# Kernel optimization log

Hardware: AMD Instinct MI355X
Metric: run time of the kernel (lower is better)

## Reference

```python
import jax, jax.numpy as jnp
import numpy as np

V = 1000      # output_dim (vocab)
H = 512       # hidden_dim
D = 512       # input_dim == d_model of MHA
HEADS = 8
DK = D // HEADS
MEM = 512     # memory_len
BS = 128      # batch
TMAX = 160    # max decode steps (== max(output_lens))


def setup_inputs() -> dict:
    key = jax.random.key(0)
    ks = jax.random.split(key, 16)
    s = 0.05
    f = lambda k, shape: jax.random.normal(k, shape, jnp.float32) * s
    memory = jax.random.normal(ks[0], (MEM, BS, D), jnp.float32)
    lens = jnp.sort(jax.random.randint(ks[1], (BS,), 1, TMAX + 1))[::-1]
    lens = lens.at[0].set(TMAX)  # torch runs max(output_lens) steps; pin to TMAX
    return dict(
        memory=memory,
        emb=f(ks[2], (V, H)),
        Wq=f(ks[3], (D, 2 * H)), bq=f(ks[4], (D,)),
        Wk=f(ks[5], (D, D)), bk=f(ks[6], (D,)),
        Wv=f(ks[7], (D, D)), bv=f(ks[8], (D,)),
        W_ih=f(ks[9], (3 * H, D)), W_hh=f(ks[10], (3 * H, H)),
        b_ih=f(ks[11], (3 * H,)), b_hh=f(ks[12], (3 * H,)),
        Wfc=f(ks[13], (V, H)), bfc=f(ks[14], (V,)),
        output_lens=lens,
    )


def _forward(memory, emb, Wq, bq, Wk, bk, Wv, bv, W_ih, W_hh, b_ih, b_hh, Wfc, bfc, output_lens):
    mem_len, bs, _ = memory.shape
    scale = 1.0 / np.sqrt(DK)
    # Precompute key/value projections once (memory is constant over decode steps).
    # (mem_len, bs, D) -> (bs, heads, mem_len, dk)
    kp = (memory @ Wk.T + bk).reshape(mem_len, bs, HEADS, DK).transpose(1, 2, 0, 3)
    vp = (memory @ Wv.T + bv).reshape(mem_len, bs, HEADS, DK).transpose(1, 2, 0, 3)

    def step(carry, i):
        out, hid = carry  # (bs, V), (bs, H)
        tok = jnp.argmax(out, axis=-1)                 # greedy feedback (annotations=None)
        q = jnp.concatenate([emb[tok], hid], axis=-1) @ Wq.T + bq  # (bs, D)
        qh = q.reshape(bs, HEADS, DK)
        att = jax.nn.softmax(jnp.einsum('bhd,bhmd->bhm', qh, kp) * scale, axis=-1)
        ctx = jnp.einsum('bhm,bhmd->bhd', att, vp).reshape(bs, D)
        # GRU cell (PyTorch gate order: r, z, n)
        gi = ctx @ W_ih.T + b_ih
        gh = hid @ W_hh.T + b_hh
        ir, iz, inn = jnp.split(gi, 3, axis=-1)
        hr, hz, hn = jnp.split(gh, 3, axis=-1)
        r = jax.nn.sigmoid(ir + hr)
        z = jax.nn.sigmoid(iz + hz)
        n = jnp.tanh(inn + r * hn)
        h_new = (1.0 - z) * n + z * hid
        o_new = h_new @ Wfc.T + bfc
        # Ragged masking: torch truncates finished batch items; each item is
        # independent, so masking the recorded outputs is equivalent.
        run = (i < output_lens)[:, None]
        ys = (jnp.where(run, o_new, 0.0),
              jnp.where(run, h_new, 0.0),
              jnp.where(run, att.mean(axis=1), 0.0))
        return (o_new, h_new), ys

    init = (jnp.zeros((bs, V), jnp.float32), jnp.zeros((bs, H), jnp.float32))
    _, (outputs, hiddens, scores) = jax.lax.scan(step, init, jnp.arange(TMAX))
    return outputs, hiddens, scores  # (T,bs,V), (T,bs,H), (T,bs,mem_len)


def reference(memory, emb, Wq, bq, Wk, bk, Wv, bv, W_ih, W_hh, b_ih, b_hh, Wfc, bfc, output_lens):
    return _forward(memory, emb, Wq, bq, Wk, bk, Wv, bv, W_ih, W_hh, b_ih, b_hh, Wfc, bfc, output_lens)
```

## Files before the change

### kernel.cpp

```cpp
#include <hip/hip_runtime.h>
#include <math.h>

__global__ __launch_bounds__(256) void kv_proj(
    const float* __restrict__ mem, const float* __restrict__ W,
    const float* __restrict__ bias, float* __restrict__ outp) {
  __shared__ float As[32][68];
  __shared__ float Bs[32][68];
  int gid = blockIdx.x;
  int jt = gid & 7, mt = (gid >> 3) & 7, b = gid >> 6;
  int t = threadIdx.x;
  int lm = t >> 2;
  int kq = (t & 3) * 8;
  int tx = t & 15, ty = t >> 4;
  float acc[4][4];
  #pragma unroll
  for (int r = 0; r < 4; ++r)
    #pragma unroll
    for (int c = 0; c < 4; ++c) acc[r][c] = 0.f;
  const float* Arow = mem + (size_t)(mt * 64 + lm) * 65536 + (size_t)b * 512 + kq;
  const float* Brow = W + (size_t)(jt * 64 + lm) * 512 + kq;
  for (int k0 = 0; k0 < 512; k0 += 32) {
    float4 a0 = *(const float4*)(Arow + k0);
    float4 a1 = *(const float4*)(Arow + k0 + 4);
    float4 b0 = *(const float4*)(Brow + k0);
    float4 b1 = *(const float4*)(Brow + k0 + 4);
    As[kq + 0][lm] = a0.x; As[kq + 1][lm] = a0.y; As[kq + 2][lm] = a0.z; As[kq + 3][lm] = a0.w;
    As[kq + 4][lm] = a1.x; As[kq + 5][lm] = a1.y; As[kq + 6][lm] = a1.z; As[kq + 7][lm] = a1.w;
    Bs[kq + 0][lm] = b0.x; Bs[kq + 1][lm] = b0.y; Bs[kq + 2][lm] = b0.z; Bs[kq + 3][lm] = b0.w;
    Bs[kq + 4][lm] = b1.x; Bs[kq + 5][lm] = b1.y; Bs[kq + 6][lm] = b1.z; Bs[kq + 7][lm] = b1.w;
    __syncthreads();
    #pragma unroll
    for (int k = 0; k < 32; ++k) {
      float4 av = *(const float4*)&As[k][ty * 4];
      float4 bv = *(const float4*)&Bs[k][tx * 4];
      float ar[4] = {av.x, av.y, av.z, av.w};
      float br[4] = {bv.x, bv.y, bv.z, bv.w};
      #pragma unroll
      for (int r = 0; r < 4; ++r)
        #pragma unroll
        for (int c = 0; c < 4; ++c) acc[r][c] = fmaf(ar[r], br[c], acc[r][c]);
    }
    __syncthreads();
  }
  float4 bb = *(const float4*)(bias + jt * 64 + tx * 4);
  #pragma unroll
  for (int r = 0; r < 4; ++r) {
    int m = mt * 64 + ty * 4 + r;
    float4 o;
    o.x = acc[r][0] + bb.x; o.y = acc[r][1] + bb.y;
    o.z = acc[r][2] + bb.z; o.w = acc[r][3] + bb.w;
    *(float4*)(outp + (((size_t)b * 8 + jt) * 512 + m) * 64 + tx * 4) = o;
  }
}

__global__ __launch_bounds__(256) void kv_projT(
    const float* __restrict__ mem, const float* __restrict__ W,
    const float* __restrict__ bias, float* __restrict__ outp) {
  __shared__ float As[32][68];
  __shared__ float Bs[32][68];
  int gid = blockIdx.x;
  int jt = gid & 7, mt = (gid >> 3) & 7, b = gid >> 6;
  int t = threadIdx.x;
  int lm = t >> 2;
  int kq = (t & 3) * 8;
  int tx = t & 15, ty = t >> 4;
  float acc[4][4];
  #pragma unroll
  for (int r = 0; r < 4; ++r)
    #pragma unroll
    for (int c = 0; c < 4; ++c) acc[r][c] = 0.f;
  const float* Arow = mem + (size_t)(mt * 64 + lm) * 65536 + (size_t)b * 512 + kq;
  const float* Brow = W + (size_t)(jt * 64 + lm) * 512 + kq;
  for (int k0 = 0; k0 < 512; k0 += 32) {
    float4 a0 = *(const float4*)(Arow + k0);
    float4 a1 = *(const float4*)(Arow + k0 + 4);
    float4 b0 = *(const float4*)(Brow + k0);
    float4 b1 = *(const float4*)(Brow + k0 + 4);
    As[kq + 0][lm] = a0.x; As[kq + 1][lm] = a0.y; As[kq + 2][lm] = a0.z; As[kq + 3][lm] = a0.w;
    As[kq + 4][lm] = a1.x; As[kq + 5][lm] = a1.y; As[kq + 6][lm] = a1.z; As[kq + 7][lm] = a1.w;
    Bs[kq + 0][lm] = b0.x; Bs[kq + 1][lm] = b0.y; Bs[kq + 2][lm] = b0.z; Bs[kq + 3][lm] = b0.w;
    Bs[kq + 4][lm] = b1.x; Bs[kq + 5][lm] = b1.y; Bs[kq + 6][lm] = b1.z; Bs[kq + 7][lm] = b1.w;
    __syncthreads();
    #pragma unroll
    for (int k = 0; k < 32; ++k) {
      float4 av = *(const float4*)&As[k][ty * 4];
      float4 bv = *(const float4*)&Bs[k][tx * 4];
      float ar[4] = {av.x, av.y, av.z, av.w};
      float br[4] = {bv.x, bv.y, bv.z, bv.w};
      #pragma unroll
      for (int r = 0; r < 4; ++r)
        #pragma unroll
        for (int c = 0; c < 4; ++c) acc[r][c] = fmaf(ar[r], br[c], acc[r][c]);
    }
    __syncthreads();
  }
  float4 bb = *(const float4*)(bias + jt * 64 + tx * 4);
  float bc[4] = {bb.x, bb.y, bb.z, bb.w};
  #pragma unroll
  for (int r = 0; r < 4; ++r) {
    int m = mt * 64 + ty * 4 + r;
    #pragma unroll
    for (int c = 0; c < 4; ++c) {
      int d = tx * 4 + c;
      outp[((size_t)(b * 8 + jt) * 64 + d) * 512 + m] = acc[r][c] + bc[c];
    }
  }
}

__global__ __launch_bounds__(256) void init_kernel(float* __restrict__ h0,
                                                   unsigned long long* __restrict__ packed) {
  int t = threadIdx.x + blockIdx.x * blockDim.x;
  for (int i = t; i < 128 * 512; i += blockDim.x * gridDim.x) h0[i] = 0.f;
  if (t < 128) packed[t] = (0x80000000ull << 32) | 0xFFFFFFFFull;
}

__global__ __launch_bounds__(256) void attn_fused(
    const float* __restrict__ kpT, const float* __restrict__ vp,
    const float* __restrict__ emb, const float* __restrict__ Wq,
    const float* __restrict__ bq, const unsigned long long* __restrict__ packed,
    const float* __restrict__ h_prev, float* __restrict__ ctx,
    float* __restrict__ att_buf) {
  int b = blockIdx.x >> 3, hd = blockIdx.x & 7;
  __shared__ float act[1024];
  __shared__ float qs[64];
  __shared__ float att[512];
  __shared__ __align__(16) float red[16][68];
  __shared__ float rmax[4], rsum[4];
  __shared__ int tok_s;
  int t = threadIdx.x;
  if (t == 0) tok_s = (int)(0xFFFFFFFFu - (unsigned int)(packed[b] & 0xFFFFFFFFull));
  __syncthreads();
  int tok = tok_s;
  act[t]       = emb[(size_t)tok * 512 + t];
  act[256 + t] = emb[(size_t)tok * 512 + 256 + t];
  act[512 + t] = h_prev[(size_t)b * 512 + t];
  act[768 + t] = h_prev[(size_t)b * 512 + 256 + t];
  __syncthreads();

  {
    int jl = t >> 2, kc = t & 3;
    const float* wrow = Wq + (size_t)(hd * 64 + jl) * 1024 + kc * 256;
    const float* a = act + kc * 256;
    float p = 0.f;
    #pragma unroll 8
    for (int i = 0; i < 256; i += 4) {
      float4 w = *(const float4*)(wrow + i);
      p = fmaf(a[i + 0], w.x, p);
      p = fmaf(a[i + 1], w.y, p);
      p = fmaf(a[i + 2], w.z, p);
      p = fmaf(a[i + 3], w.w, p);
    }
    p += __shfl_xor(p, 1);
    p += __shfl_xor(p, 2);
    if (kc == 0) qs[jl] = p + bq[hd * 64 + jl];
  }
  __syncthreads();

  const float* Kb = kpT + (size_t)(b * 8 + hd) * 32768;
  float s0 = 0.f, s1 = 0.f;
  {
    int m2 = 2 * t;
    #pragma unroll 8
    for (int d = 0; d < 64; ++d) {
      float2 kk = *(const float2*)(Kb + (size_t)d * 512 + m2);
      float qd = qs[d];
      s0 = fmaf(qd, kk.x, s0);
      s1 = fmaf(qd, kk.y, s1);
    }
    s0 *= 0.125f;
    s1 *= 0.125f;
  }
  float mx = fmaxf(s0, s1);
  #pragma unroll
  for (int o = 32; o > 0; o >>= 1) mx = fmaxf(mx, __shfl_xor(mx, o));
  if ((t & 63) == 0) rmax[t >> 6] = mx;
  __syncthreads();
  mx = fmaxf(fmaxf(rmax[0], rmax[1]), fmaxf(rmax[2], rmax[3]));
  float e0 = expf(s0 - mx), e1 = expf(s1 - mx);
  float sm = e0 + e1;
  #pragma unroll
  for (int o = 32; o > 0; o >>= 1) sm += __shfl_xor(sm, o);
  if ((t & 63) == 0) rsum[t >> 6] = sm;
  __syncthreads();
  sm = rsum[0] + rsum[1] + rsum[2] + rsum[3];
  float inv = 1.f / sm;
  float a0 = e0 * inv, a1 = e1 * inv;
  att[2 * t] = a0;
  att[2 * t + 1] = a1;
  *(float2*)(att_buf + (size_t)(b * 8 + hd) * 512 + 2 * t) = make_float2(a0, a1);
  __syncthreads();

  const float* Vb = vp + (size_t)(b * 8 + hd) * 32768;
  {
    int dsl = (t & 15) * 4, g = t >> 4;
    float c0 = 0.f, c1 = 0.f, c2 = 0.f, c3 = 0.f;
    #pragma unroll 4
    for (int m = g; m < 512; m += 16) {
      float4 vv = *(const float4*)(Vb + (size_t)m * 64 + dsl);
      float am = att[m];
      c0 = fmaf(am, vv.x, c0);
      c1 = fmaf(am, vv.y, c1);
      c2 = fmaf(am, vv.z, c2);
      c3 = fmaf(am, vv.w, c3);
    }
    red[g][dsl + 0] = c0;
    red[g][dsl + 1] = c1;
    red[g][dsl + 2] = c2;
    red[g][dsl + 3] = c3;
  }
  __syncthreads();
  if (t < 64) {
    float cc = 0.f;
    #pragma unroll
    for (int g2 = 0; g2 < 16; ++g2) cc += red[g2][t];
    ctx[(size_t)b * 512 + hd * 64 + t] = cc;
  }
}

__global__ __launch_bounds__(256) void gru_kernel(
    const float* __restrict__ W_ih, const float* __restrict__ W_hh,
    const float* __restrict__ b_ih, const float* __restrict__ b_hh,
    const float* __restrict__ ctx, const float* __restrict__ h_prev,
    float* __restrict__ h_new, const float* __restrict__ att_buf,
    const int* __restrict__ lens, float* __restrict__ out_hid,
    float* __restrict__ out_sc, unsigned long long* __restrict__ packed,
    int step) {
  __shared__ float cs[8][512];
  __shared__ float hs[8][512];
  int bi = blockIdx.x;
  int t = threadIdx.x;
  if (bi >= 256) {
    int sb = bi - 256;
    if (sb == 0 && t < 128) packed[t] = 0ull;
    #pragma unroll
    for (int i = 0; i < 4; ++i) {
      int flat = sb * 1024 + i * 256 + t;
      int bb = flat >> 9, m = flat & 511;
      float sum = 0.f;
      #pragma unroll
      for (int h = 0; h < 8; ++h) sum += att_buf[(size_t)(bb * 8 + h) * 512 + m];
      float val = sum * 0.125f;
      out_sc[(size_t)step * 65536 + flat] = (step < lens[bb]) ? val : 0.f;
    }
    return;
  }
  int bt = bi >> 4, jt = bi & 15;
  #pragma unroll
  for (int i = 0; i < 16; ++i) {
    int flat = i * 256 + t;
    int lb = flat >> 9, k = flat & 511;
    cs[lb][k] = ctx[(size_t)(bt * 8 + lb) * 512 + k];
    hs[lb][k] = h_prev[(size_t)(bt * 8 + lb) * 512 + k];
  }
  __syncthreads();
  int lb = t >> 5, j = (jt << 5) + (t & 31);
  int b = bt * 8 + lb;
  float air = b_ih[j], aiz = b_ih[512 + j], ain = b_ih[1024 + j];
  float ahr = b_hh[j], ahz = b_hh[512 + j], ahn = b_hh[1024 + j];
  const float* c = cs[lb];
  const float* hh = hs[lb];
  const float* wi0 = W_ih + (size_t)j * 512;
  const float* wi1 = W_ih + (size_t)(512 + j) * 512;
  const float* wi2 = W_ih + (size_t)(1024 + j) * 512;
  const float* wh0 = W_hh + (size_t)j * 512;
  const float* wh1 = W_hh + (size_t)(512 + j) * 512;
  const float* wh2 = W_hh + (size_t)(1024 + j) * 512;
  #pragma unroll 2
  for (int k = 0; k < 512; k += 4) {
    float4 wa = *(const float4*)(wi0 + k);
    float4 wb = *(const float4*)(wi1 + k);
    float4 wc = *(const float4*)(wi2 + k);
    float4 wd = *(const float4*)(wh0 + k);
    float4 we = *(const float4*)(wh1 + k);
    float4 wf = *(const float4*)(wh2 + k);
    float c0 = c[k], c1 = c[k + 1], c2 = c[k + 2], c3 = c[k + 3];
    float h0 = hh[k], h1 = hh[k + 1], h2 = hh[k + 2], h3 = hh[k + 3];
    air = fmaf(c0, wa.x, air); air = fmaf(c1, wa.y, air); air = fmaf(c2, wa.z, air); air = fmaf(c3, wa.w, air);
    aiz = fmaf(c0, wb.x, aiz); aiz = fmaf(c1, wb.y, aiz); aiz = fmaf(c2, wb.z, aiz); aiz = fmaf(c3, wb.w, aiz);
    ain = fmaf(c0, wc.x, ain); ain = fmaf(c1, wc.y, ain); ain = fmaf(c2, wc.z, ain); ain = fmaf(c3, wc.w, ain);
    ahr = fmaf(h0, wd.x, ahr); ahr = fmaf(h1, wd.y, ahr); ahr = fmaf(h2, wd.z, ahr); ahr = fmaf(h3, wd.w, ahr);
    ahz = fmaf(h0, we.x, ahz); ahz = fmaf(h1, we.y, ahz); ahz = fmaf(h2, we.z, ahz); ahz = fmaf(h3, we.w, ahz);
    ahn = fmaf(h0, wf.x, ahn); ahn = fmaf(h1, wf.y, ahn); ahn = fmaf(h2, wf.z, ahn); ahn = fmaf(h3, wf.w, ahn);
  }
  float r = 1.f / (1.f + expf(-(air + ahr)));
  float z = 1.f / (1.f + expf(-(aiz + ahz)));
  float n = tanhf(fmaf(r, ahn, ain));
  float hp = hh[j];
  float hv = (1.f - z) * n + z * hp;
  h_new[(size_t)b * 512 + j] = hv;
  out_hid[(size_t)step * 65536 + (size_t)b * 512 + j] = (step < lens[b]) ? hv : 0.f;
}

__global__ __launch_bounds__(256) void logits_kernel(
    const float* __restrict__ Wfc, const float* __restrict__ bfc,
    const float* __restrict__ h_new, const int* __restrict__ lens,
    float* __restrict__ out_o, unsigned long long* __restrict__ packed,
    int step) {
  __shared__ float hs[8][512];
  int bi = blockIdx.x;
  int t = threadIdx.x;
  int bt = bi >> 4, vt = bi & 15;
  #pragma unroll
  for (int i = 0; i < 16; ++i) {
    int flat = i * 256 + t;
    int lb = flat >> 9, k = flat & 511;
    hs[lb][k] = h_new[(size_t)(bt * 8 + lb) * 512 + k];
  }
  __syncthreads();
  int lb = t >> 5, vv = t & 31;
  int b = bt * 8 + lb;
  const float* a = hs[lb];
  int run = step < lens[b];
  float bestv = -1e30f;
  int besti = 0;
  #pragma unroll
  for (int r = 0; r < 2; ++r) {
    int v = vt * 64 + r * 32 + vv;
    if (v < 1000) {
      float acc = bfc[v];
      const float* wrow = Wfc + (size_t)v * 512;
      #pragma unroll 4
      for (int k = 0; k < 512; k += 4) {
        float4 w = *(const float4*)(wrow + k);
        acc = fmaf(a[k + 0], w.x, acc);
        acc = fmaf(a[k + 1], w.y, acc);
        acc = fmaf(a[k + 2], w.z, acc);
        acc = fmaf(a[k + 3], w.w, acc);
      }
      out_o[(size_t)step * 128000 + (size_t)b * 1000 + v] = run ? acc : 0.f;
      if (acc > bestv) { bestv = acc; besti = v; }
    }
  }
  #pragma unroll
  for (int o = 16; o > 0; o >>= 1) {
    float ov = __shfl_xor(bestv, o);
    int oi = __shfl_xor(besti, o);
    if (ov > bestv || (ov == bestv && oi < besti)) { bestv = ov; besti = oi; }
  }
  if (vv == 0) {
    unsigned int fb = __float_as_uint(bestv);
    fb = (fb & 0x80000000u) ? ~fb : (fb | 0x80000000u);
    unsigned long long key =
        ((unsigned long long)fb << 32) | (unsigned long long)(0xFFFFFFFFu - (unsigned int)besti);
    atomicMax(packed + b, key);
  }
}

extern "C" void kernel_launch(void* const* d_in, const int* in_sizes, int n_in,
                              void* d_out, int out_size, void* d_ws, size_t ws_size,
                              hipStream_t stream) {
  const float* memory = (const float*)d_in[0];
  const float* emb    = (const float*)d_in[1];
  const float* Wq     = (const float*)d_in[2];
  const float* bq     = (const float*)d_in[3];
  const float* Wk     = (const float*)d_in[4];
  const float* bk     = (const float*)d_in[5];
  const float* Wv     = (const float*)d_in[6];
  const float* bv     = (const float*)d_in[7];
  const float* W_ih   = (const float*)d_in[8];
  const float* W_hh   = (const float*)d_in[9];
  const float* b_ih   = (const float*)d_in[10];
  const float* b_hh   = (const float*)d_in[11];
  const float* Wfc    = (const float*)d_in[12];
  const float* bfc    = (const float*)d_in[13];
  const int* lens     = (const int*)d_in[14];

  float* ws = (float*)d_ws;
  float* kpT     = ws;
  float* vp      = kpT + 33554432;
  float* ctx     = vp + 33554432;
  float* h0      = ctx + 65536;
  float* h1      = h0 + 65536;
  float* att_buf = h1 + 65536;
  unsigned long long* packed = (unsigned long long*)(att_buf + 524288);

  float* out   = (float*)d_out;
  float* out_o = out;
  float* out_h = out + 20480000;
  float* out_s = out_h + 10485760;

  kv_projT<<<8192, 256, 0, stream>>>(memory, Wk, bk, kpT);
  kv_proj<<<8192, 256, 0, stream>>>(memory, Wv, bv, vp);
  init_kernel<<<64, 256, 0, stream>>>(h0, packed);

  for (int t = 0; t < 160; ++t) {
    float* hp = (t & 1) ? h1 : h0;
    float* hn = (t & 1) ? h0 : h1;
    attn_fused<<<1024, 256, 0, stream>>>(kpT, vp, emb, Wq, bq, packed, hp, ctx, att_buf);
    gru_kernel<<<320, 256, 0, stream>>>(W_ih, W_hh, b_ih, b_hh, ctx, hp, hn,
                                        att_buf, lens, out_h, out_s, packed, t);
    logits_kernel<<<256, 256, 0, stream>>>(Wfc, bfc, hn, lens, out_o, packed, t);
  }
}
```

Measured before the change: 31.53 ms.

## Store K/V projections in fp16 and precompute embedding query table

K and V projections are now stored as half precision, which halves the per-step bandwidth attention needs to stream them. The embedding half of the query projection is precomputed once as a vocab-by-D table (E2 = emb·Wq_emb + bq). The hidden half of the query is computed inside the logits kernel for the next step, so the attention kernel just adds two vectors instead of running a 1024-wide matvec per block. This trades accuracy (fp16 K/V rounding) and extra logits-kernel work for much less memory traffic in attention.

```diff
diff --git a/kernel.cpp b/kernel.cpp
--- a/kernel.cpp
+++ b/kernel.cpp
@@ -1,9 +1,10 @@
 #include <hip/hip_runtime.h>
+#include <hip/hip_fp16.h>
 #include <math.h>
 
 __global__ __launch_bounds__(256) void kv_proj(
     const float* __restrict__ mem, const float* __restrict__ W,
-    const float* __restrict__ bias, float* __restrict__ outp) {
+    const float* __restrict__ bias, __half* __restrict__ outp) {
   __shared__ float As[32][68];
   __shared__ float Bs[32][68];
   int gid = blockIdx.x;
@@ -46,16 +47,17 @@
   #pragma unroll
   for (int r = 0; r < 4; ++r) {
     int m = mt * 64 + ty * 4 + r;
-    float4 o;
-    o.x = acc[r][0] + bb.x; o.y = acc[r][1] + bb.y;
-    o.z = acc[r][2] + bb.z; o.w = acc[r][3] + bb.w;
-    *(float4*)(outp + (((size_t)b * 8 + jt) * 512 + m) * 64 + tx * 4) = o;
+    __half2 p0 = __floats2half2_rn(acc[r][0] + bb.x, acc[r][1] + bb.y);
+    __half2 p1 = __floats2half2_rn(acc[r][2] + bb.z, acc[r][3] + bb.w);
+    union { uint2 u; __half2 h[2]; } W2;
+    W2.h[0] = p0; W2.h[1] = p1;
+    *(uint2*)(outp + (((size_t)b * 8 + jt) * 512 + m) * 64 + tx * 4) = W2.u;
   }
 }
 
 __global__ __launch_bounds__(256) void kv_projT(
     const float* __restrict__ mem, const float* __restrict__ W,
-    const float* __restrict__ bias, float* __restrict__ outp) {
+    const float* __restrict__ bias, __half* __restrict__ outp) {
   __shared__ float As[32][68];
   __shared__ float Bs[32][68];
   int gid = blockIdx.x;
@@ -102,26 +104,90 @@
     #pragma unroll
     for (int c = 0; c < 4; ++c) {
       int d = tx * 4 + c;
-      outp[((size_t)(b * 8 + jt) * 64 + d) * 512 + m] = acc[r][c] + bc[c];
+      outp[((size_t)(b * 8 + jt) * 64 + d) * 512 + m] = __float2half_rn(acc[r][c] + bc[c]);
+    }
+  }
+}
+
+__global__ __launch_bounds__(256) void e2_kernel(
+    const float* __restrict__ emb, const float* __restrict__ Wq,
+    const float* __restrict__ bq, float* __restrict__ E2) {
+  __shared__ float As[32][68];
+  __shared__ float Bs[32][68];
+  int gid = blockIdx.x;
+  int jt = gid & 7, mt = gid >> 3;
+  int t = threadIdx.x;
+  int lm = t >> 2;
+  int kq = (t & 3) * 8;
+  int tx = t & 15, ty = t >> 4;
+  float acc[4][4];
+  #pragma unroll
+  for (int r = 0; r < 4; ++r)
+    #pragma unroll
+    for (int c = 0; c < 4; ++c) acc[r][c] = 0.f;
+  int v = mt * 64 + lm;
+  bool aok = v < 1000;
+  const float* Arow = emb + (size_t)v * 512 + kq;
+  const float* Brow = Wq + (size_t)(jt * 64 + lm) * 1024 + kq;
+  for (int k0 = 0; k0 < 512; k0 += 32) {
+    float4 a0, a1;
+    if (aok) {
+      a0 = *(const float4*)(Arow + k0);
+      a1 = *(const float4*)(Arow + k0 + 4);
+    } else {
+      a0 = make_float4(0.f, 0.f, 0.f, 0.f);
+      a1 = make_float4(0.f, 0.f, 0.f, 0.f);
+    }
+    float4 b0 = *(const float4*)(Brow + k0);
+    float4 b1 = *(const float4*)(Brow + k0 + 4);
+    As[kq + 0][lm] = a0.x; As[kq + 1][lm] = a0.y; As[kq + 2][lm] = a0.z; As[kq + 3][lm] = a0.w;
+    As[kq + 4][lm] = a1.x; As[kq + 5][lm] = a1.y; As[kq + 6][lm] = a1.z; As[kq + 7][lm] = a1.w;
+    Bs[kq + 0][lm] = b0.x; Bs[kq + 1][lm] = b0.y; Bs[kq + 2][lm] = b0.z; Bs[kq + 3][lm] = b0.w;
+    Bs[kq + 4][lm] = b1.x; Bs[kq + 5][lm] = b1.y; Bs[kq + 6][lm] = b1.z; Bs[kq + 7][lm] = b1.w;
+    __syncthreads();
+    #pragma unroll
+    for (int k = 0; k < 32; ++k) {
+      float4 av = *(const float4*)&As[k][ty * 4];
+      float4 bv = *(const float4*)&Bs[k][tx * 4];
+      float ar[4] = {av.x, av.y, av.z, av.w};
+      float br[4] = {bv.x, bv.y, bv.z, bv.w};
+      #pragma unroll
+      for (int r = 0; r < 4; ++r)
+        #pragma unroll
+        for (int c = 0; c < 4; ++c) acc[r][c] = fmaf(ar[r], br[c], acc[r][c]);
+    }
+    __syncthreads();
+  }
+  float4 bb = *(const float4*)(bq + jt * 64 + tx * 4);
+  float bc[4] = {bb.x, bb.y, bb.z, bb.w};
+  #pragma unroll
+  for (int r = 0; r < 4; ++r) {
+    int vv = mt * 64 + ty * 4 + r;
+    if (vv < 1000) {
+      #pragma unroll
+      for (int c = 0; c < 4; ++c)
+        E2[(size_t)vv * 512 + jt * 64 + tx * 4 + c] = acc[r][c] + bc[c];
     }
   }
 }
 
 __global__ __launch_bounds__(256) void init_kernel(float* __restrict__ h0,
+                                                   float* __restrict__ qh,
                                                    unsigned long long* __restrict__ packed) {
   int t = threadIdx.x + blockIdx.x * blockDim.x;
-  for (int i = t; i < 128 * 512; i += blockDim.x * gridDim.x) h0[i] = 0.f;
+  for (int i = t; i < 128 * 512; i += blockDim.x * gridDim.x) {
+    h0[i] = 0.f;
+    qh[i] = 0.f;
+  }
   if (t < 128) packed[t] = (0x80000000ull << 32) | 0xFFFFFFFFull;
 }
 
 __global__ __launch_bounds__(256) void attn_fused(
-    const float* __restrict__ kpT, const float* __restrict__ vp,
-    const float* __restrict__ emb, const float* __restrict__ Wq,
-    const float* __restrict__ bq, const unsigned long long* __restrict__ packed,
-    const float* __restrict__ h_prev, float* __restrict__ ctx,
-    float* __restrict__ att_buf) {
+    const __half* __restrict__ kpT, const __half* __restrict__ vp,
+    const float* __restrict__ E2, const float* __restrict__ qh,
+    const unsigned long long* __restrict__ packed,
+    float* __restrict__ ctx, float* __restrict__ att_buf) {
   int b = blockIdx.x >> 3, hd = blockIdx.x & 7;
-  __shared__ float act[1024];
   __shared__ float qs[64];
   __shared__ float att[512];
   __shared__ __align__(16) float red[16][68];
@@ -131,41 +197,21 @@
   if (t == 0) tok_s = (int)(0xFFFFFFFFu - (unsigned int)(packed[b] & 0xFFFFFFFFull));
   __syncthreads();
   int tok = tok_s;
-  act[t]       = emb[(size_t)tok * 512 + t];
-  act[256 + t] = emb[(size_t)tok * 512 + 256 + t];
-  act[512 + t] = h_prev[(size_t)b * 512 + t];
-  act[768 + t] = h_prev[(size_t)b * 512 + 256 + t];
-  __syncthreads();
-
-  {
-    int jl = t >> 2, kc = t & 3;
-    const float* wrow = Wq + (size_t)(hd * 64 + jl) * 1024 + kc * 256;
-    const float* a = act + kc * 256;
-    float p = 0.f;
-    #pragma unroll 8
-    for (int i = 0; i < 256; i += 4) {
-      float4 w = *(const float4*)(wrow + i);
-      p = fmaf(a[i + 0], w.x, p);
-      p = fmaf(a[i + 1], w.y, p);
-      p = fmaf(a[i + 2], w.z, p);
-      p = fmaf(a[i + 3], w.w, p);
-    }
-    p += __shfl_xor(p, 1);
-    p += __shfl_xor(p, 2);
-    if (kc == 0) qs[jl] = p + bq[hd * 64 + jl];
-  }
-  __syncthreads();
-
-  const float* Kb = kpT + (size_t)(b * 8 + hd) * 32768;
+  if (t < 64)
+    qs[t] = qh[(size_t)b * 512 + hd * 64 + t] + E2[(size_t)tok * 512 + hd * 64 + t];
+  __syncthreads();
+
+  const __half* Kb = kpT + (size_t)(b * 8 + hd) * 32768;
   float s0 = 0.f, s1 = 0.f;
   {
     int m2 = 2 * t;
-    #pragma unroll 8
+    #pragma unroll 16
     for (int d = 0; d < 64; ++d) {
-      float2 kk = *(const float2*)(Kb + (size_t)d * 512 + m2);
+      __half2 kk = *(const __half2*)(Kb + (size_t)d * 512 + m2);
+      float2 kf = __half22float2(kk);
       float qd = qs[d];
-      s0 = fmaf(qd, kk.x, s0);
-      s1 = fmaf(qd, kk.y, s1);
+      s0 = fmaf(qd, kf.x, s0);
+      s1 = fmaf(qd, kf.y, s1);
     }
     s0 *= 0.125f;
     s1 *= 0.125f;
@@ -190,18 +236,21 @@
   *(float2*)(att_buf + (size_t)(b * 8 + hd) * 512 + 2 * t) = make_float2(a0, a1);
   __syncthreads();
 
-  const float* Vb = vp + (size_t)(b * 8 + hd) * 32768;
+  const __half* Vb = vp + (size_t)(b * 8 + hd) * 32768;
   {
     int dsl = (t & 15) * 4, g = t >> 4;
     float c0 = 0.f, c1 = 0.f, c2 = 0.f, c3 = 0.f;
-    #pragma unroll 4
+    #pragma unroll 8
     for (int m = g; m < 512; m += 16) {
-      float4 vv = *(const float4*)(Vb + (size_t)m * 64 + dsl);
+      union { uint2 u; __half2 h[2]; } U;
+      U.u = *(const uint2*)(Vb + (size_t)m * 64 + dsl);
+      float2 f01 = __half22float2(U.h[0]);
+      float2 f23 = __half22float2(U.h[1]);
       float am = att[m];
-      c0 = fmaf(am, vv.x, c0);
-      c1 = fmaf(am, vv.y, c1);
-      c2 = fmaf(am, vv.z, c2);
-      c3 = fmaf(am, vv.w, c3);
+      c0 = fmaf(am, f01.x, c0);
+      c1 = fmaf(am, f01.y, c1);
+      c2 = fmaf(am, f23.x, c2);
+      c3 = fmaf(am, f23.y, c3);
     }
     red[g][dsl + 0] = c0;
     red[g][dsl + 1] = c1;
@@ -295,7 +344,7 @@
     const float* __restrict__ Wfc, const float* __restrict__ bfc,
     const float* __restrict__ h_new, const int* __restrict__ lens,
     float* __restrict__ out_o, unsigned long long* __restrict__ packed,
-    int step) {
+    const float* __restrict__ Wq, float* __restrict__ qh, int step) {
   __shared__ float hs[8][512];
   int bi = blockIdx.x;
   int t = threadIdx.x;
@@ -343,6 +392,21 @@
     unsigned long long key =
         ((unsigned long long)fb << 32) | (unsigned long long)(0xFFFFFFFFu - (unsigned int)besti);
     atomicMax(packed + b, key);
+  }
+
+  {
+    int jq = vt * 32 + (t & 31);
+    const float* wrow = Wq + (size_t)jq * 1024 + 512;
+    float acc = 0.f;
+    #pragma unroll 4
+    for (int k = 0; k < 512; k += 4) {
+      float4 w = *(const float4*)(wrow + k);
+      acc = fmaf(a[k + 0], w.x, acc);
+      acc = fmaf(a[k + 1], w.y, acc);
+      acc = fmaf(a[k + 2], w.z, acc);
+      acc = fmaf(a[k + 3], w.w, acc);
+    }
+    qh[(size_t)b * 512 + jq] = acc;
   }
 }
 
@@ -365,13 +429,14 @@
   const float* bfc    = (const float*)d_in[13];
   const int* lens     = (const int*)d_in[14];
 
-  float* ws = (float*)d_ws;
-  float* kpT     = ws;
-  float* vp      = kpT + 33554432;
-  float* ctx     = vp + 33554432;
+  __half* kpT = (__half*)d_ws;
+  __half* vp  = kpT + 33554432;
+  float* ctx     = (float*)(vp + 33554432);
   float* h0      = ctx + 65536;
   float* h1      = h0 + 65536;
-  float* att_buf = h1 + 65536;
+  float* qh      = h1 + 65536;
+  float* E2      = qh + 65536;
+  float* att_buf = E2 + 512000;
   unsigned long long* packed = (unsigned long long*)(att_buf + 524288);
 
   float* out   = (float*)d_out;
@@ -381,14 +446,15 @@
 
   kv_projT<<<8192, 256, 0, stream>>>(memory, Wk, bk, kpT);
   kv_proj<<<8192, 256, 0, stream>>>(memory, Wv, bv, vp);
-  init_kernel<<<64, 256, 0, stream>>>(h0, packed);
+  e2_kernel<<<128, 256, 0, stream>>>(emb, Wq, bq, E2);
+  init_kernel<<<64, 256, 0, stream>>>(h0, qh, packed);
 
   for (int t = 0; t < 160; ++t) {
     float* hp = (t & 1) ? h1 : h0;
     float* hn = (t & 1) ? h0 : h1;
-    attn_fused<<<1024, 256, 0, stream>>>(kpT, vp, emb, Wq, bq, packed, hp, ctx, att_buf);
+    attn_fused<<<1024, 256, 0, stream>>>(kpT, vp, E2, qh, packed, ctx, att_buf);
     gru_kernel<<<320, 256, 0, stream>>>(W_ih, W_hh, b_ih, b_hh, ctx, hp, hn,
                                         att_buf, lens, out_h, out_s, packed, t);
-    logits_kernel<<<256, 256, 0, stream>>>(Wfc, bfc, hn, lens, out_o, packed, t);
-  }
-}
+    logits_kernel<<<256, 256, 0, stream>>>(Wfc, bfc, hn, lens, out_o, packed, Wq, qh, t);
+  }
+}
```

Measured after the change: 25.94 ms. 1.22x faster.
